# Performance work log

Measured on AMD Instinct MI355X. Metric: run time of the kernel, lower is better.

Reference implementation:

```python
import jax, jax.numpy as jnp
import numpy as np

VOCAB = 128
EMB = 16
HID = 512
B, T = 128, 1024


def setup_inputs() -> dict:
    key = jax.random.key(0)
    ks = jax.random.split(key, 8)
    s = 0.05
    return {
        "x": jax.random.randint(ks[0], (B, T), 0, VOCAB),
        "emb": jax.random.normal(ks[1], (VOCAB, EMB), jnp.float32) * s,
        "W_ih": jax.random.normal(ks[2], (HID, EMB), jnp.float32) * s,
        "W_hh": jax.random.normal(ks[3], (HID, HID), jnp.float32) * s,
        "b_ih": jax.random.normal(ks[4], (HID,), jnp.float32) * s,
        "b_hh": jax.random.normal(ks[5], (HID,), jnp.float32) * s,
        "W_fc": jax.random.normal(ks[6], (VOCAB, HID), jnp.float32) * s,
        "b_fc": jax.random.normal(ks[7], (VOCAB,), jnp.float32) * s,
    }


def reference(x, emb, W_ih, W_hh, b_ih, b_hh, W_fc, b_fc):
    # Embedding lookup: [B, T, EMB]
    xe = emb[x]
    # Precompute input-to-hidden part for all steps: [B, T, HID]
    xp = jnp.einsum('bte,he->bth', xe, W_ih) + b_ih + b_hh
    h0 = jnp.zeros((xe.shape[0], W_hh.shape[0]), xe.dtype)

    def step(h, xt):  # xt: [B, HID]
        h_new = jnp.tanh(xt + h @ W_hh.T)
        return h_new, h_new

    # scan over time: [T, B, HID]
    _, hs = jax.lax.scan(step, h0, jnp.swapaxes(xp, 0, 1))
    hs = jnp.swapaxes(hs, 0, 1)  # [B, T, HID]
    logits = jnp.einsum('bth,vh->btv', hs, W_fc) + b_fc  # [B, T, VOCAB]
    return logits
```

## Files before the change

kernel.cpp:

```cpp
#include <hip/hip_runtime.h>
#include <cstdint>


typedef short bf16x8 __attribute__((ext_vector_type(8)));
typedef float f32x4 __attribute__((ext_vector_type(4)));

#define VOCAB 128
#define EMB   16
#define HID   512
#define TT    1024
#define NCL   8
#define BB    16
#define JC    32
#define NWG   128
#define BUFW  (NCL * BB * HID)
#define CNTOFF (2 * BUFW)
#define PJC   33

__device__ __forceinline__ unsigned short f2bf(float f) {
  uint32_t u = __builtin_bit_cast(uint32_t, f);
  u += 0x7FFFu + ((u >> 16) & 1u);
  return (unsigned short)(u >> 16);
}
__device__ __forceinline__ float bf2f(unsigned short s) {
  uint32_t u = (uint32_t)s << 16;
  return __builtin_bit_cast(float, u);
}
__device__ __forceinline__ float ftanh(float z) {
  z = fminf(15.f, fmaxf(-15.f, z));
  float e = __expf(2.f * z);
  return (e - 1.f) * __builtin_amdgcn_rcpf(e + 1.f);
}
__device__ __forceinline__ uint32_t aload(const uint32_t* p) {
  return __hip_atomic_load(p, __ATOMIC_RELAXED, __HIP_MEMORY_SCOPE_AGENT);
}
__device__ __forceinline__ void astore(uint32_t* p, uint32_t v) {
  __hip_atomic_store(p, v, __ATOMIC_RELAXED, __HIP_MEMORY_SCOPE_AGENT);
}

__global__ __launch_bounds__(256, 1) void charrnn_kernel(
    const int* __restrict__ xin,
    const float* __restrict__ emb,
    const float* __restrict__ wih,
    const float* __restrict__ whh,
    const float* __restrict__ bih,
    const float* __restrict__ bhh,
    const float* __restrict__ wfc,
    const float* __restrict__ bfc,
    float* __restrict__ out,
    uint32_t* __restrict__ hx)
{
  __shared__ __align__(16) unsigned short a_hi[16 * 512];
  __shared__ __align__(16) unsigned short a_lo[16 * 512];
  __shared__ float ep[VOCAB * PJC];
  __shared__ unsigned char xtok[BB * TT];
  __shared__ __align__(16) float red[2][256];

  const int tid  = threadIdx.x;
  const int wave = tid >> 6;
  const int lane = tid & 63;
  const int col  = lane & 15;
  const int quad = lane >> 4;
  const int cl   = blockIdx.x & 7;
  const int m    = blockIdx.x >> 3;

  bf16x8 wfh[16], wfl[16], wfcf[8];
  if (wave < 2) {
    const int nrow = m * JC + wave * 16 + col;
    const float* wr = whh + (size_t)nrow * HID + quad * 8;
    #pragma unroll
    for (int ks = 0; ks < 16; ++ks) {
      bf16x8 hi, lo;
      #pragma unroll
      for (int j = 0; j < 8; ++j) {
        float w = wr[ks * 32 + j];
        unsigned short h = f2bf(w);
        hi[j] = (short)h;
        lo[j] = (short)f2bf(w - bf2f(h));
      }
      wfh[ks] = hi; wfl[ks] = lo;
    }
  } else {
    const int vrow = m * 8 + (col & 7);
    const float* wr = wfc + (size_t)vrow * HID + (wave - 2) * 256 + quad * 8;
    #pragma unroll
    for (int ks = 0; ks < 8; ++ks) {
      bf16x8 f;
      #pragma unroll
      for (int j = 0; j < 8; ++j) f[j] = (short)f2bf(wr[ks * 32 + j]);
      wfcf[ks] = f;
    }
  }
  const float bfcr = bfc[m * 8 + (col & 7)];

  for (int i = tid; i < 16 * 512; i += 256) { a_hi[i] = 0; a_lo[i] = 0; }
  for (int i = tid; i < VOCAB * JC; i += 256) {
    int v = i >> 5, jl = i & 31;
    int jg = m * JC + jl;
    float s = bih[jg] + bhh[jg];
    #pragma unroll
    for (int e = 0; e < EMB; ++e) s += emb[v * EMB + e] * wih[jg * EMB + e];
    ep[v * PJC + jl] = s;
  }
  for (int i = tid; i < BB * TT; i += 256) {
    int b = i >> 10, t = i & 1023;
    xtok[i] = (unsigned char)xin[(cl * BB + b) * TT + t];
  }
  __syncthreads();

  const int lw = tid & 31;
  const int r0 = tid >> 5;
  const float rcp20 = 1.f / 1048576.f;
  uint32_t* const cnt = hx + CNTOFF + cl * 32;
  f32x4 prev_lacc = {0.f, 0.f, 0.f, 0.f};

  #pragma unroll 1
  for (int t = 0; t <= TT + 1; ++t) {
    const int par = t & 1;
    const uint32_t tag = (uint32_t)t & 0x7FFu;
    uint32_t* const p0 = hx + par * BUFW + (cl * BB + r0) * HID + lw;
    uint32_t* const p1 = p0 + 8 * HID;

    if (wave >= 2 && t >= 2) {
      *(f32x4*)&red[wave - 2][lane * 4] = prev_lacc;
    }

    if (t >= 1 && t <= TT) {
      const uint32_t target = 32u * (uint32_t)t;
      while ((int32_t)(aload(cnt) - target) < 0) {}

      const int qk = lw >> 3, jj = lw & 7;
      const int idx0 = ((qk << 4) + r0) * 8 + jj;
      const int idx1 = idx0 + 64;
      for (;;) {
        uint32_t v0[16], v1[16];
        #pragma unroll
        for (int i = 0; i < 16; ++i) v0[i] = aload(p0 + 32 * i);
        #pragma unroll
        for (int i = 0; i < 16; ++i) v1[i] = aload(p1 + 32 * i);
        uint32_t bad = 0;
        #pragma unroll
        for (int i = 0; i < 16; ++i) bad |= (v0[i] ^ tag) | (v1[i] ^ tag);
        if ((bad & 0x7FFu) == 0) {
          #pragma unroll
          for (int i = 0; i < 16; ++i) {
            float h0 = (float)(((int)v0[i]) >> 11) * rcp20;
            uint32_t uh0 = __builtin_bit_cast(uint32_t, h0) & 0xFFFF0000u;
            float l0 = h0 - __builtin_bit_cast(float, uh0);
            a_hi[i * 512 + idx0] = (unsigned short)(uh0 >> 16);
            a_lo[i * 512 + idx0] = (unsigned short)(__builtin_bit_cast(uint32_t, l0) >> 16);
            float h1 = (float)(((int)v1[i]) >> 11) * rcp20;
            uint32_t uh1 = __builtin_bit_cast(uint32_t, h1) & 0xFFFF0000u;
            float l1 = h1 - __builtin_bit_cast(float, uh1);
            a_hi[i * 512 + idx1] = (unsigned short)(uh1 >> 16);
            a_lo[i * 512 + idx1] = (unsigned short)(__builtin_bit_cast(uint32_t, l1) >> 16);
          }
          break;
        }
      }
    }
    __syncthreads();

    if (wave < 2) {
      if (t < TT) {
        f32x4 acc0 = {0.f,0.f,0.f,0.f}, acc1 = {0.f,0.f,0.f,0.f}, acc2 = {0.f,0.f,0.f,0.f};
        #pragma unroll
        for (int ks = 0; ks < 16; ++ks) {
          bf16x8 ah = *(const bf16x8*)&a_hi[ks * 512 + lane * 8];
          bf16x8 al = *(const bf16x8*)&a_lo[ks * 512 + lane * 8];
          acc0 = __builtin_amdgcn_mfma_f32_16x16x32_bf16(ah, wfh[ks], acc0, 0, 0, 0);
          acc1 = __builtin_amdgcn_mfma_f32_16x16x32_bf16(al, wfh[ks], acc1, 0, 0, 0);
          acc2 = __builtin_amdgcn_mfma_f32_16x16x32_bf16(ah, wfl[ks], acc2, 0, 0, 0);
        }
        const int jl = wave * 16 + col;
        const uint32_t ntag = (uint32_t)(t + 1) & 0x7FFu;
        uint32_t* wb = hx + ((t + 1) & 1) * BUFW + (cl * BB) * HID + m * JC + jl;
        #pragma unroll
        for (int i = 0; i < 4; ++i) {
          const int b = quad * 4 + i;
          float z = acc0[i] + acc1[i] + acc2[i]
                  + ep[(int)xtok[b * TT + t] * PJC + jl];
          float h = ftanh(z);
          int q = __float2int_rn(h * 1048576.f);
          q = max(min(q, 1048575), -1048576);
          astore(wb + b * HID, ((uint32_t)q << 11) | ntag);
        }
        if (lane == 0)
          (void)__hip_atomic_fetch_add(cnt, 1u, __ATOMIC_RELAXED,
                                       __HIP_MEMORY_SCOPE_AGENT);
      }
    } else {
      if (wave == 2 && t >= 2 && col < 8) {
        #pragma unroll
        for (int i = 0; i < 4; ++i) {
          const int b = quad * 4 + i;
          float s = red[0][lane * 4 + i] + red[1][lane * 4 + i] + bfcr;
          out[((size_t)(cl * BB + b) * TT + (t - 2)) * VOCAB + m * 8 + col] = s;
        }
      }
      if (t >= 1 && t <= TT) {
        f32x4 lacc = {0.f, 0.f, 0.f, 0.f};
        const int kb = (wave - 2) * 8;
        #pragma unroll
        for (int ks = 0; ks < 8; ++ks) {
          bf16x8 ah = *(const bf16x8*)&a_hi[(kb + ks) * 512 + lane * 8];
          bf16x8 al = *(const bf16x8*)&a_lo[(kb + ks) * 512 + lane * 8];
          lacc = __builtin_amdgcn_mfma_f32_16x16x32_bf16(ah, wfcf[ks], lacc, 0, 0, 0);
          lacc = __builtin_amdgcn_mfma_f32_16x16x32_bf16(al, wfcf[ks], lacc, 0, 0, 0);
        }
        prev_lacc = lacc;
      }
    }
    __syncthreads();
  }
}

extern "C" void kernel_launch(void* const* d_in, const int* in_sizes, int n_in,
                              void* d_out, int out_size, void* d_ws, size_t ws_size,
                              hipStream_t stream) {
  (void)in_sizes; (void)n_in; (void)out_size;
  if (ws_size < (size_t)CNTOFF * sizeof(uint32_t) + 4096) return;

  const int*   x    = (const int*)d_in[0];
  const float* embp = (const float*)d_in[1];
  const float* W_ih = (const float*)d_in[2];
  const float* W_hh = (const float*)d_in[3];
  const float* b_ih = (const float*)d_in[4];
  const float* b_hh = (const float*)d_in[5];
  const float* W_fc = (const float*)d_in[6];
  const float* b_fc = (const float*)d_in[7];

  hipMemsetAsync((uint32_t*)d_ws + CNTOFF, 0, NCL * 32 * sizeof(uint32_t), stream);

  charrnn_kernel<<<NWG, 256, 0, stream>>>(x, embp, W_ih, W_hh, b_ih, b_hh, W_fc, b_fc,
                                          (float*)d_out, (uint32_t*)d_ws);
}
```

Measured before the change: 3.288 ms.

## Replace shared atomic counter with per-wave flags and vectorize hidden-state sweep

Each producer wave now stores its own release flag with the step number, replacing the atomic fetch-add on one shared counter. Consumer lanes each poll one flag with an acquire load. The hidden-state gather now reads rows with 16-byte vector loads, re-polling with atomic loads only if tags are stale, and writes 4-wide packed bf16 values into a padded LDS layout (stride 520) to cut bank conflicts. The aim is less contention on a single atomic and fewer, wider memory transactions per step. The risk is that the initial non-atomic vector loads could be served stale data from cache.

```diff
diff --git a/kernel.cpp b/kernel.cpp
--- a/kernel.cpp
+++ b/kernel.cpp
@@ -4,6 +4,7 @@
 
 typedef short bf16x8 __attribute__((ext_vector_type(8)));
 typedef float f32x4 __attribute__((ext_vector_type(4)));
+typedef unsigned short u16x4 __attribute__((ext_vector_type(4)));
 
 #define VOCAB 128
 #define EMB   16
@@ -14,8 +15,9 @@
 #define JC    32
 #define NWG   128
 #define BUFW  (NCL * BB * HID)
-#define CNTOFF (2 * BUFW)
+#define FLGOFF (2 * BUFW)
 #define PJC   33
+#define CS    520
 
 __device__ __forceinline__ unsigned short f2bf(float f) {
   uint32_t u = __builtin_bit_cast(uint32_t, f);
@@ -36,6 +38,47 @@
 }
 __device__ __forceinline__ void astore(uint32_t* p, uint32_t v) {
   __hip_atomic_store(p, v, __ATOMIC_RELAXED, __HIP_MEMORY_SCOPE_AGENT);
+}
+
+__device__ __forceinline__ void sweep_row(const uint32_t* prow, int lw, int row,
+                                          uint32_t tag,
+                                          unsigned short* a_hi,
+                                          unsigned short* a_lo) {
+  uint32_t w[16];
+  const uint4* pv = (const uint4*)(prow + lw * 4);
+  uint4 q0 = pv[0], q1 = pv[32], q2 = pv[64], q3 = pv[96];
+  w[0]=q0.x; w[1]=q0.y; w[2]=q0.z; w[3]=q0.w;
+  w[4]=q1.x; w[5]=q1.y; w[6]=q1.z; w[7]=q1.w;
+  w[8]=q2.x; w[9]=q2.y; w[10]=q2.z; w[11]=q2.w;
+  w[12]=q3.x; w[13]=q3.y; w[14]=q3.z; w[15]=q3.w;
+  uint32_t bad = 0;
+  #pragma unroll
+  for (int i = 0; i < 16; ++i) bad |= (w[i] ^ tag);
+  while (bad & 0x7FFu) {
+    bad = 0;
+    #pragma unroll
+    for (int i = 0; i < 16; ++i) {
+      w[i] = aload(prow + lw * 4 + (i >> 2) * 128 + (i & 3));
+      bad |= (w[i] ^ tag);
+    }
+  }
+  const float rcp20 = 1.f / 1048576.f;
+  const int qk = (lw >> 1) & 3, jh = (lw & 1) * 4, ksb = lw >> 3;
+  #pragma unroll
+  for (int i = 0; i < 4; ++i) {
+    const int sa = (i * 4 + ksb) * CS + (qk * 16 + row) * 8 + jh;
+    u16x4 hv, lv;
+    #pragma unroll
+    for (int q = 0; q < 4; ++q) {
+      float h = (float)(((int)w[i * 4 + q]) >> 11) * rcp20;
+      uint32_t uh = __builtin_bit_cast(uint32_t, h) & 0xFFFF0000u;
+      float l = h - __builtin_bit_cast(float, uh);
+      hv[q] = (unsigned short)(uh >> 16);
+      lv[q] = (unsigned short)(__builtin_bit_cast(uint32_t, l) >> 16);
+    }
+    *(u16x4*)&a_hi[sa] = hv;
+    *(u16x4*)&a_lo[sa] = lv;
+  }
 }
 
 __global__ __launch_bounds__(256, 1) void charrnn_kernel(
@@ -50,8 +93,8 @@
     float* __restrict__ out,
     uint32_t* __restrict__ hx)
 {
-  __shared__ __align__(16) unsigned short a_hi[16 * 512];
-  __shared__ __align__(16) unsigned short a_lo[16 * 512];
+  __shared__ __align__(16) unsigned short a_hi[16 * CS];
+  __shared__ __align__(16) unsigned short a_lo[16 * CS];
   __shared__ float ep[VOCAB * PJC];
   __shared__ unsigned char xtok[BB * TT];
   __shared__ __align__(16) float red[2][256];
@@ -93,7 +136,7 @@
   }
   const float bfcr = bfc[m * 8 + (col & 7)];
 
-  for (int i = tid; i < 16 * 512; i += 256) { a_hi[i] = 0; a_lo[i] = 0; }
+  for (int i = tid; i < 16 * CS; i += 256) { a_hi[i] = 0; a_lo[i] = 0; }
   for (int i = tid; i < VOCAB * JC; i += 256) {
     int v = i >> 5, jl = i & 31;
     int jg = m * JC + jl;
@@ -110,54 +153,26 @@
 
   const int lw = tid & 31;
   const int r0 = tid >> 5;
-  const float rcp20 = 1.f / 1048576.f;
-  uint32_t* const cnt = hx + CNTOFF + cl * 32;
+  uint32_t* const flags = hx + FLGOFF + cl * 32;
   f32x4 prev_lacc = {0.f, 0.f, 0.f, 0.f};
 
   #pragma unroll 1
   for (int t = 0; t <= TT + 1; ++t) {
     const int par = t & 1;
     const uint32_t tag = (uint32_t)t & 0x7FFu;
-    uint32_t* const p0 = hx + par * BUFW + (cl * BB + r0) * HID + lw;
-    uint32_t* const p1 = p0 + 8 * HID;
+    const uint32_t* const p0 = hx + par * BUFW + (cl * BB + r0) * HID;
+    const uint32_t* const p1 = p0 + 8 * HID;
 
     if (wave >= 2 && t >= 2) {
       *(f32x4*)&red[wave - 2][lane * 4] = prev_lacc;
     }
 
     if (t >= 1 && t <= TT) {
-      const uint32_t target = 32u * (uint32_t)t;
-      while ((int32_t)(aload(cnt) - target) < 0) {}
-
-      const int qk = lw >> 3, jj = lw & 7;
-      const int idx0 = ((qk << 4) + r0) * 8 + jj;
-      const int idx1 = idx0 + 64;
-      for (;;) {
-        uint32_t v0[16], v1[16];
-        #pragma unroll
-        for (int i = 0; i < 16; ++i) v0[i] = aload(p0 + 32 * i);
-        #pragma unroll
-        for (int i = 0; i < 16; ++i) v1[i] = aload(p1 + 32 * i);
-        uint32_t bad = 0;
-        #pragma unroll
-        for (int i = 0; i < 16; ++i) bad |= (v0[i] ^ tag) | (v1[i] ^ tag);
-        if ((bad & 0x7FFu) == 0) {
-          #pragma unroll
-          for (int i = 0; i < 16; ++i) {
-            float h0 = (float)(((int)v0[i]) >> 11) * rcp20;
-            uint32_t uh0 = __builtin_bit_cast(uint32_t, h0) & 0xFFFF0000u;
-            float l0 = h0 - __builtin_bit_cast(float, uh0);
-            a_hi[i * 512 + idx0] = (unsigned short)(uh0 >> 16);
-            a_lo[i * 512 + idx0] = (unsigned short)(__builtin_bit_cast(uint32_t, l0) >> 16);
-            float h1 = (float)(((int)v1[i]) >> 11) * rcp20;
-            uint32_t uh1 = __builtin_bit_cast(uint32_t, h1) & 0xFFFF0000u;
-            float l1 = h1 - __builtin_bit_cast(float, uh1);
-            a_hi[i * 512 + idx1] = (unsigned short)(uh1 >> 16);
-            a_lo[i * 512 + idx1] = (unsigned short)(__builtin_bit_cast(uint32_t, l1) >> 16);
-          }
-          break;
-        }
-      }
+      const int fl = lane & 31;
+      while ((int32_t)(aload(flags + fl) - (uint32_t)t) < 0) {}
+      (void)__hip_atomic_load(flags + fl, __ATOMIC_ACQUIRE, __HIP_MEMORY_SCOPE_AGENT);
+      sweep_row(p0, lw, r0,     tag, a_hi, a_lo);
+      sweep_row(p1, lw, r0 + 8, tag, a_hi, a_lo);
     }
     __syncthreads();
 
@@ -166,8 +181,8 @@
         f32x4 acc0 = {0.f,0.f,0.f,0.f}, acc1 = {0.f,0.f,0.f,0.f}, acc2 = {0.f,0.f,0.f,0.f};
         #pragma unroll
         for (int ks = 0; ks < 16; ++ks) {
-          bf16x8 ah = *(const bf16x8*)&a_hi[ks * 512 + lane * 8];
-          bf16x8 al = *(const bf16x8*)&a_lo[ks * 512 + lane * 8];
+          bf16x8 ah = *(const bf16x8*)&a_hi[ks * CS + lane * 8];
+          bf16x8 al = *(const bf16x8*)&a_lo[ks * CS + lane * 8];
           acc0 = __builtin_amdgcn_mfma_f32_16x16x32_bf16(ah, wfh[ks], acc0, 0, 0, 0);
           acc1 = __builtin_amdgcn_mfma_f32_16x16x32_bf16(al, wfh[ks], acc1, 0, 0, 0);
           acc2 = __builtin_amdgcn_mfma_f32_16x16x32_bf16(ah, wfl[ks], acc2, 0, 0, 0);
@@ -186,8 +201,8 @@
           astore(wb + b * HID, ((uint32_t)q << 11) | ntag);
         }
         if (lane == 0)
-          (void)__hip_atomic_fetch_add(cnt, 1u, __ATOMIC_RELAXED,
-                                       __HIP_MEMORY_SCOPE_AGENT);
+          __hip_atomic_store(flags + (m * 2 + wave), (uint32_t)(t + 1),
+                             __ATOMIC_RELEASE, __HIP_MEMORY_SCOPE_AGENT);
       }
     } else {
       if (wave == 2 && t >= 2 && col < 8) {
@@ -203,8 +218,8 @@
         const int kb = (wave - 2) * 8;
         #pragma unroll
         for (int ks = 0; ks < 8; ++ks) {
-          bf16x8 ah = *(const bf16x8*)&a_hi[(kb + ks) * 512 + lane * 8];
-          bf16x8 al = *(const bf16x8*)&a_lo[(kb + ks) * 512 + lane * 8];
+          bf16x8 ah = *(const bf16x8*)&a_hi[(kb + ks) * CS + lane * 8];
+          bf16x8 al = *(const bf16x8*)&a_lo[(kb + ks) * CS + lane * 8];
           lacc = __builtin_amdgcn_mfma_f32_16x16x32_bf16(ah, wfcf[ks], lacc, 0, 0, 0);
           lacc = __builtin_amdgcn_mfma_f32_16x16x32_bf16(al, wfcf[ks], lacc, 0, 0, 0);
         }
@@ -219,7 +234,7 @@
                               void* d_out, int out_size, void* d_ws, size_t ws_size,
                               hipStream_t stream) {
   (void)in_sizes; (void)n_in; (void)out_size;
-  if (ws_size < (size_t)CNTOFF * sizeof(uint32_t) + 4096) return;
+  if (ws_size < (size_t)FLGOFF * sizeof(uint32_t) + 4096) return;
 
   const int*   x    = (const int*)d_in[0];
   const float* embp = (const float*)d_in[1];
@@ -230,7 +245,7 @@
   const float* W_fc = (const float*)d_in[6];
   const float* b_fc = (const float*)d_in[7];
 
-  hipMemsetAsync((uint32_t*)d_ws + CNTOFF, 0, NCL * 32 * sizeof(uint32_t), stream);
+  hipMemsetAsync((uint32_t*)d_ws + FLGOFF, 0, NCL * 32 * sizeof(uint32_t), stream);
 
   charrnn_kernel<<<NWG, 256, 0, stream>>>(x, embp, W_ih, W_hh, b_ih, b_hh, W_fc, b_fc,
                                           (float*)d_out, (uint32_t*)d_ws);
```

Measured after the change: 8.320 ms. 2.53x slower.
